# Kernel optimization log

Hardware: AMD Instinct MI355X
Metric: run time of the kernel (lower is better)

Reference implementation:

```python
import jax, jax.numpy as jnp
import numpy as np

DIM = 768
HEADS = 12
FF = 3072
EPS = 1e-6


def setup_inputs() -> dict:
    key = jax.random.key(0)
    ks = jax.random.split(key, 12)
    B, S, D, F_ = 64, 197, DIM, FF
    s = 0.02
    inp = {
        "x": jax.random.normal(ks[0], (B, S, D), jnp.float32),
        "Wq": jax.random.normal(ks[1], (D, D), jnp.float32) * s,
        "bq": jnp.zeros((D,), jnp.float32),
        "Wk": jax.random.normal(ks[2], (D, D), jnp.float32) * s,
        "bk": jnp.zeros((D,), jnp.float32),
        "Wv": jax.random.normal(ks[3], (D, D), jnp.float32) * s,
        "bv": jnp.zeros((D,), jnp.float32),
        "Wo": jax.random.normal(ks[4], (D, D), jnp.float32) * s,
        "bo": jnp.zeros((D,), jnp.float32),
        "ln1_w": jnp.ones((D,), jnp.float32),
        "ln1_b": jnp.zeros((D,), jnp.float32),
        "W1": jax.random.normal(ks[5], (D, F_), jnp.float32) * s,
        "b1": jnp.zeros((F_,), jnp.float32),
        "W2": jax.random.normal(ks[6], (F_, D), jnp.float32) * s,
        "b2": jnp.zeros((D,), jnp.float32),
        "ln2_w": jnp.ones((D,), jnp.float32),
        "ln2_b": jnp.zeros((D,), jnp.float32),
        "mask": jnp.ones((B, S), jnp.int32),
    }
    return inp


def _layernorm(x, w, b):
    m = jnp.mean(x, axis=-1, keepdims=True)
    v = jnp.mean(jnp.square(x - m), axis=-1, keepdims=True)  # unbiased=False
    return (x - m) / jnp.sqrt(v + EPS) * w + b


def _block(x, mask_f, Wq, bq, Wk, bk, Wv, bv, Wo, bo, ln1_w, ln1_b, W1, b1, W2, b2, ln2_w, ln2_b):
    B, S, D = x.shape
    H = HEADS
    Dh = D // H
    # --- attention (pre-norm) ---
    h = _layernorm(x, ln1_w, ln1_b)
    q = (h @ Wq + bq).reshape(B, S, H, Dh).transpose(0, 2, 1, 3)
    k = (h @ Wk + bk).reshape(B, S, H, Dh).transpose(0, 2, 1, 3)
    v = (h @ Wv + bv).reshape(B, S, H, Dh).transpose(0, 2, 1, 3)
    scores = jnp.einsum("bhqd,bhkd->bhqk", q, k) / jnp.sqrt(jnp.float32(Dh))
    scores = scores - 10000.0 * (1.0 - mask_f[:, None, None, :])
    probs = jax.nn.softmax(scores, axis=-1)
    attn = jnp.einsum("bhqk,bhkd->bhqd", probs, v).transpose(0, 2, 1, 3).reshape(B, S, D)
    x = x + (attn @ Wo + bo)  # dropout = identity (eval)
    # --- FFN (pre-norm), exact erf GELU (F.gelu default) ---
    h = _layernorm(x, ln2_w, ln2_b)
    h = jax.nn.gelu(h @ W1 + b1, approximate=False)
    x = x + (h @ W2 + b2)
    return x


def reference(x, Wq, bq, Wk, bk, Wv, bv, Wo, bo, ln1_w, ln1_b, W1, b1, W2, b2, ln2_w, ln2_b, mask):
    mask_f = mask.astype(jnp.float32)
    return _block(x, mask_f, Wq, bq, Wk, bk, Wv, bv, Wo, bo, ln1_w, ln1_b, W1, b1, W2, b2, ln2_w, ln2_b)
```

## Files before the change

### kernel.cpp

```cpp
#include <hip/hip_runtime.h>
#include <stdint.h>

#define B_   64
#define S_   197
#define D_   768
#define H_   12
#define F_   3072
#define BS_  (B_ * S_)

typedef __attribute__((ext_vector_type(8))) short short8;
typedef __attribute__((ext_vector_type(4))) float f32x4;

__device__ __forceinline__ float bf2f(unsigned short h) {
    union { unsigned int u; float f; } v; v.u = ((unsigned int)h) << 16; return v.f;
}
__device__ __forceinline__ unsigned short f2bf(float f) {
    union { float f; unsigned int u; } v; v.f = f;
    unsigned int r = v.u + 0x7FFFu + ((v.u >> 16) & 1u);
    return (unsigned short)(r >> 16);
}

__device__ __forceinline__ void g2l16(const void* g, void* l) {
    __builtin_amdgcn_global_load_lds(
        (const __attribute__((address_space(1))) unsigned int*)g,
        (__attribute__((address_space(3))) unsigned int*)l, 16, 0, 0);
}

__global__ __launch_bounds__(256)
void transpose_all(const float* __restrict__ Wq, const float* __restrict__ Wk,
                   const float* __restrict__ Wv, const float* __restrict__ Wo,
                   const float* __restrict__ W1, const float* __restrict__ W2,
                   const float* __restrict__ bq, const float* __restrict__ bk,
                   const float* __restrict__ bv,
                   unsigned short* __restrict__ wqkvT, unsigned short* __restrict__ woT,
                   unsigned short* __restrict__ w1T, unsigned short* __restrict__ w2T,
                   float* __restrict__ bcat) {
    int blk = blockIdx.x;
    int tx = threadIdx.x, ty = threadIdx.y;
    if (blk == 6912) {
        for (int i = ty * 32 + tx; i < 2304; i += 256)
            bcat[i] = i < 768 ? bq[i] : (i < 1536 ? bk[i - 768] : bv[i - 1536]);
        return;
    }
    const float* W; unsigned short* Wt; int K, N, rel, nx;
    if (blk < 2304) {
        int m = blk / 576; rel = blk - m * 576; K = 768; N = 768; nx = 24;
        W  = m == 0 ? Wq : m == 1 ? Wk : m == 2 ? Wv : Wo;
        Wt = m < 3 ? wqkvT + (size_t)m * 768 * 768 : woT;
    } else if (blk < 4608) {
        rel = blk - 2304; K = 768; N = 3072; nx = 96; W = W1; Wt = w1T;
    } else {
        rel = blk - 4608; K = 3072; N = 768; nx = 24; W = W2; Wt = w2T;
    }
    int n0 = (rel % nx) * 32, k0 = (rel / nx) * 32;
    __shared__ float t[32][33];
#pragma unroll
    for (int i = ty; i < 32; i += 8) t[i][tx] = W[(size_t)(k0 + i) * N + n0 + tx];
    __syncthreads();
#pragma unroll
    for (int i = ty; i < 32; i += 8) Wt[(size_t)(n0 + i) * K + k0 + tx] = f2bf(t[tx][i]);
}

__global__ __launch_bounds__(256)
void ln_kernel(const float* __restrict__ x, const float* __restrict__ w,
               const float* __restrict__ b, unsigned short* __restrict__ out) {
    int row = blockIdx.x; size_t base = (size_t)row * 768;
    int tid = threadIdx.x;
    float v0 = x[base + tid], v1 = x[base + tid + 256], v2 = x[base + tid + 512];
    float s1 = v0 + v1 + v2;
    float s2 = v0 * v0 + v1 * v1 + v2 * v2;
#pragma unroll
    for (int off = 32; off > 0; off >>= 1) { s1 += __shfl_xor(s1, off); s2 += __shfl_xor(s2, off); }
    __shared__ float sa[4], sb[4];
    int w4 = tid >> 6;
    if ((tid & 63) == 0) { sa[w4] = s1; sb[w4] = s2; }
    __syncthreads();
    s1 = sa[0] + sa[1] + sa[2] + sa[3];
    s2 = sb[0] + sb[1] + sb[2] + sb[3];
    float mean = s1 * (1.f / 768.f);
    float var  = s2 * (1.f / 768.f) - mean * mean;
    float rstd = rsqrtf(var + 1e-6f);
    out[base + tid]       = f2bf((v0 - mean) * rstd * w[tid]       + b[tid]);
    out[base + tid + 256] = f2bf((v1 - mean) * rstd * w[tid + 256] + b[tid + 256]);
    out[base + tid + 512] = f2bf((v2 - mean) * rstd * w[tid + 512] + b[tid + 512]);
}

template<int MODE>
__global__ __launch_bounds__(256)
void gemm_bf16(const unsigned short* __restrict__ A, const unsigned short* __restrict__ Bt,
               const float* __restrict__ bias, const float* __restrict__ resid,
               void* __restrict__ out, int M, int N, int K) {
    __shared__ unsigned short As[2][128 * 32];
    __shared__ unsigned short Bs[2][128 * 32];
    const int tid = threadIdx.x;
    const int l = tid & 63, w = tid >> 6;
    const int lr = l & 15, lg = l >> 4;
    const int wr = w >> 1, wc = w & 1;

    const int nMt = gridDim.y;
    const int nwg = gridDim.x * gridDim.y;
    const int orig = blockIdx.x + gridDim.x * blockIdx.y;
    const int q8 = nwg >> 3, r8 = nwg & 7;
    const int xcd = orig & 7, idx = orig >> 3;
    const int wgid = (xcd < r8 ? xcd * (q8 + 1) : r8 * (q8 + 1) + (xcd - r8) * q8) + idx;
    const int bm0 = (wgid % nMt) * 128;
    const int bn0 = (wgid / nMt) * 128;

    const int srow = l >> 2;
    const int sblk = (l & 3) ^ ((l >> 3) & 3);
    auto stage = [&](int buf, int k0) {
#pragma unroll
        for (int p = 0; p < 2; ++p) {
            int r0 = p * 64 + w * 16;
            int ra = bm0 + r0 + srow; ra = ra < M ? ra : M - 1;
            g2l16(A + (size_t)ra * K + k0 + sblk * 8, &As[buf][r0 * 32]);
            int rb = bn0 + r0 + srow;
            g2l16(Bt + (size_t)rb * K + k0 + sblk * 8, &Bs[buf][r0 * 32]);
        }
    };

    f32x4 acc[4][4];
#pragma unroll
    for (int i = 0; i < 4; ++i)
#pragma unroll
        for (int j = 0; j < 4; ++j) acc[i][j] = (f32x4){0.f, 0.f, 0.f, 0.f};

    stage(0, 0);
    __syncthreads();
    int cur = 0;
    const int NK = K >> 5;
    const int rblk = lg ^ ((lr >> 1) & 3);
    for (int kt = 0; kt < NK; ++kt) {
        if (kt + 1 < NK) stage(cur ^ 1, (kt + 1) << 5);
        short8 af[4], bfr[4];
#pragma unroll
        for (int i = 0; i < 4; ++i) af[i]  = *(const short8*)&As[cur][(wr * 64 + i * 16 + lr) * 32 + rblk * 8];
#pragma unroll
        for (int j = 0; j < 4; ++j) bfr[j] = *(const short8*)&Bs[cur][(wc * 64 + j * 16 + lr) * 32 + rblk * 8];
#pragma unroll
        for (int i = 0; i < 4; ++i)
#pragma unroll
            for (int j = 0; j < 4; ++j)
                acc[i][j] = __builtin_amdgcn_mfma_f32_16x16x32_bf16(af[i], bfr[j], acc[i][j], 0, 0, 0);
        __syncthreads();
        cur ^= 1;
    }
#pragma unroll
    for (int i = 0; i < 4; ++i)
#pragma unroll
        for (int j = 0; j < 4; ++j)
#pragma unroll
            for (int r = 0; r < 4; ++r) {
                int gm = bm0 + wr * 64 + i * 16 + lg * 4 + r;
                int gn = bn0 + wc * 64 + j * 16 + lr;
                if (gm < M) {
                    float c = acc[i][j][r] + bias[gn];
                    if (MODE == 0) {
                        if (gn < 768) c *= 0.125f;
                        ((unsigned short*)out)[(size_t)gm * N + gn] = f2bf(c);
                    } else if (MODE == 1) {
                        ((float*)out)[(size_t)gm * N + gn] = c + resid[(size_t)gm * N + gn];
                    } else {
                        float g = 0.5f * c * (1.f + erff(c * 0.70710678118f));
                        ((unsigned short*)out)[(size_t)gm * N + gn] = f2bf(g);
                    }
                }
            }
}

__global__ __launch_bounds__(256)
void attn_mfma(const unsigned short* __restrict__ qkv, const int* __restrict__ mask,
               unsigned short* __restrict__ ctx) {
    __shared__ unsigned short Ks[208 * 64];
    __shared__ unsigned short Vt[64 * 256];
    __shared__ unsigned short Psl[4][16 * 40];
    __shared__ float maskadj[224];
    const int bh = blockIdx.x, b = bh / 12, h = bh - b * 12;
    const int tid = threadIdx.x, l = tid & 63, w = tid >> 6;
    const int lr = l & 15, lg = l >> 4;
    const unsigned short* Qg = qkv + (size_t)b * 197 * 2304 + h * 64;
    const unsigned short* Kg = Qg + 768;
    const unsigned short* Vg = Qg + 1536;

    if (tid < 224)
        maskadj[tid] = tid < 197 ? -10000.f * (1.f - (float)mask[b * 197 + tid]) : -1e30f;

    for (int c = w; c < 26; c += 4) {
        int row = c * 8 + (l >> 3);
        int rc = row < 197 ? row : 196;
        int blk = (l & 7) ^ (row & 7);
        g2l16(Kg + (size_t)rc * 2304 + blk * 8, &Ks[c * 8 * 64]);
    }
    {
        int jj = tid >> 3, db = tid & 7;
#pragma unroll
        for (int it = 0; it < 7; ++it) {
            int j = it * 32 + jj;
            short8 v = (short8){0, 0, 0, 0, 0, 0, 0, 0};
            if (j < 197) v = *(const short8*)(Vg + (size_t)j * 2304 + db * 8);
#pragma unroll
            for (int e = 0; e < 8; ++e) {
                int d = db * 8 + e;
                Vt[d * 256 + (((j >> 3) ^ (d & 7)) * 8) + (j & 7)] = (unsigned short)v[e];
            }
        }
    }
    __syncthreads();

    for (int t = w; t < 13; t += 4) {
        const int q0 = t * 16;
        int qr = q0 + lr; qr = qr < 197 ? qr : 196;
        const short8 qf0 = *(const short8*)(Qg + (size_t)qr * 2304 + lg * 8);
        const short8 qf1 = *(const short8*)(Qg + (size_t)qr * 2304 + 32 + lg * 8);

        f32x4 sc[13];
#pragma unroll
        for (int kt = 0; kt < 13; ++kt) {
            const int krow = kt * 16 + lr;
            const short8 kf0 = *(const short8*)&Ks[krow * 64 + ((lg ^ (lr & 7)) * 8)];
            const short8 kf1 = *(const short8*)&Ks[krow * 64 + (((4 + lg) ^ (lr & 7)) * 8)];
            f32x4 a = (f32x4){0.f, 0.f, 0.f, 0.f};
            a = __builtin_amdgcn_mfma_f32_16x16x32_bf16(qf0, kf0, a, 0, 0, 0);
            a = __builtin_amdgcn_mfma_f32_16x16x32_bf16(qf1, kf1, a, 0, 0, 0);
            sc[kt] = a;
        }
        float mx[4] = {-1e30f, -1e30f, -1e30f, -1e30f};
#pragma unroll
        for (int kt = 0; kt < 13; ++kt) {
            float ma = maskadj[kt * 16 + lr];
#pragma unroll
            for (int r = 0; r < 4; ++r) {
                sc[kt][r] += ma;
                mx[r] = fmaxf(mx[r], sc[kt][r]);
            }
        }
#pragma unroll
        for (int r = 0; r < 4; ++r) {
            mx[r] = fmaxf(mx[r], __shfl_xor(mx[r], 1));
            mx[r] = fmaxf(mx[r], __shfl_xor(mx[r], 2));
            mx[r] = fmaxf(mx[r], __shfl_xor(mx[r], 4));
            mx[r] = fmaxf(mx[r], __shfl_xor(mx[r], 8));
        }
        float sm[4] = {0.f, 0.f, 0.f, 0.f};
#pragma unroll
        for (int kt = 0; kt < 13; ++kt)
#pragma unroll
            for (int r = 0; r < 4; ++r) {
                float p = __expf(sc[kt][r] - mx[r]);
                sc[kt][r] = p;
                sm[r] += p;
            }
#pragma unroll
        for (int r = 0; r < 4; ++r) {
            sm[r] += __shfl_xor(sm[r], 1);
            sm[r] += __shfl_xor(sm[r], 2);
            sm[r] += __shfl_xor(sm[r], 4);
            sm[r] += __shfl_xor(sm[r], 8);
            sm[r] = 1.f / sm[r];
        }
        f32x4 ao[4];
#pragma unroll
        for (int dt = 0; dt < 4; ++dt) ao[dt] = (f32x4){0.f, 0.f, 0.f, 0.f};
        unsigned short* Pw = &Psl[w][0];
#pragma unroll
        for (int ks = 0; ks < 7; ++ks) {
#pragma unroll
            for (int tl = 0; tl < 2; ++tl) {
                const int kt = ks * 2 + tl;
#pragma unroll
                for (int r = 0; r < 4; ++r) {
                    unsigned short pv = 0;
                    if (kt < 13) pv = f2bf(sc[kt][r] * sm[r]);
                    Pw[(lg * 4 + r) * 40 + tl * 16 + lr] = pv;
                }
            }
            const short8 pf = *(const short8*)&Pw[lr * 40 + lg * 8];
#pragma unroll
            for (int dt = 0; dt < 4; ++dt) {
                const int drow = dt * 16 + lr;
                const short8 vf = *(const short8*)&Vt[drow * 256 + (((4 * ks + lg) ^ (lr & 7)) * 8)];
                ao[dt] = __builtin_amdgcn_mfma_f32_16x16x32_bf16(vf, pf, ao[dt], 0, 0, 0);
            }
        }
        const int q = q0 + lr;
        if (q < 197) {
            unsigned short* crow = ctx + ((size_t)b * 197 + q) * 768 + h * 64;
#pragma unroll
            for (int dt = 0; dt < 4; ++dt) {
                union { unsigned short u[4]; uint2 v; } pk;
#pragma unroll
                for (int r = 0; r < 4; ++r) pk.u[r] = f2bf(ao[dt][r]);
                *(uint2*)(crow + dt * 16 + lg * 4) = pk.v;
            }
        }
    }
}

extern "C" void kernel_launch(void* const* d_in, const int* in_sizes, int n_in,
                              void* d_out, int out_size, void* d_ws, size_t ws_size,
                              hipStream_t stream) {
    const float* x    = (const float*)d_in[0];
    const float* Wq   = (const float*)d_in[1];
    const float* bq   = (const float*)d_in[2];
    const float* Wk   = (const float*)d_in[3];
    const float* bk   = (const float*)d_in[4];
    const float* Wv   = (const float*)d_in[5];
    const float* bv   = (const float*)d_in[6];
    const float* Wo   = (const float*)d_in[7];
    const float* bo   = (const float*)d_in[8];
    const float* ln1w = (const float*)d_in[9];
    const float* ln1b = (const float*)d_in[10];
    const float* W1   = (const float*)d_in[11];
    const float* b1   = (const float*)d_in[12];
    const float* W2   = (const float*)d_in[13];
    const float* b2   = (const float*)d_in[14];
    const float* ln2w = (const float*)d_in[15];
    const float* ln2b = (const float*)d_in[16];
    const int*   mask = (const int*)d_in[17];

    size_t off = 0;
    auto nxt = [&](size_t bytes) -> void* {
        void* r = (char*)d_ws + off; off += (bytes + 255) & ~(size_t)255; return r;
    };
    unsigned short* hbuf  = (unsigned short*)nxt((size_t)BS_ * 768 * 2);
    unsigned short* qkvg  = (unsigned short*)nxt((size_t)BS_ * 3072 * 2);
    unsigned short* wqkvT = (unsigned short*)nxt((size_t)2304 * 768 * 2);
    unsigned short* woT   = (unsigned short*)nxt((size_t)768 * 768 * 2);
    unsigned short* w1T   = (unsigned short*)nxt((size_t)3072 * 768 * 2);
    unsigned short* w2T   = (unsigned short*)nxt((size_t)768 * 3072 * 2);
    float*          bcat  = (float*)nxt(2304 * 4);
    unsigned short* ctx   = (unsigned short*)nxt((size_t)BS_ * 768 * 2);
    (void)ws_size; (void)in_sizes; (void)n_in; (void)out_size;

    transpose_all<<<6913, dim3(32, 8), 0, stream>>>(Wq, Wk, Wv, Wo, W1, W2, bq, bk, bv,
                                                    wqkvT, woT, w1T, w2T, bcat);
    ln_kernel<<<BS_, 256, 0, stream>>>(x, ln1w, ln1b, hbuf);
    gemm_bf16<0><<<dim3(18, 99), 256, 0, stream>>>(hbuf, wqkvT, bcat, nullptr, qkvg, BS_, 2304, 768);
    attn_mfma<<<768, 256, 0, stream>>>(qkvg, mask, ctx);
    gemm_bf16<1><<<dim3(6, 99), 256, 0, stream>>>(ctx, woT, bo, x, d_out, BS_, 768, 768);
    ln_kernel<<<BS_, 256, 0, stream>>>((const float*)d_out, ln2w, ln2b, hbuf);
    gemm_bf16<2><<<dim3(24, 99), 256, 0, stream>>>(hbuf, w1T, b1, nullptr, qkvg, BS_, 3072, 768);
    gemm_bf16<1><<<dim3(6, 99), 256, 0, stream>>>(qkvg, w2T, b2, (const float*)d_out, d_out, BS_, 768, 3072);
}
```

Before: 482.8 us.

## Replace 128x128 GEMM with 256x256 tile, 512-thread, BK=64 pipelined kernel

Replaces the 128x128x32 bf16 GEMM with a 256x256x64 tile kernel using 8 waves. Each wave computes 128x64 of the output, and global-to-LDS prefetch of the next K tile is interleaved with MFMA sub-steps, with priority hints and a wider XOR swizzle. Larger tiles are meant to raise data reuse and cut LDS and barrier overhead per FLOP. The cost is 128KB LDS per block, so only one block fits per CU despite launch_bounds(512,2). Grids also shrink (e.g. 150 blocks for the N=768 GEMMs), which can underfill 256 CUs. The exact erff in the FFN GELU epilogue is swapped for an Abramowitz-Stegun polynomial approximation.

```diff
diff --git a/kernel.cpp b/kernel.cpp
--- a/kernel.cpp
+++ b/kernel.cpp
@@ -24,6 +24,16 @@
     __builtin_amdgcn_global_load_lds(
         (const __attribute__((address_space(1))) unsigned int*)g,
         (__attribute__((address_space(3))) unsigned int*)l, 16, 0, 0);
+}
+
+__device__ __forceinline__ float gelu_f(float c) {
+    float z = fabsf(c) * 0.70710678118f;
+    float t = __builtin_amdgcn_rcpf(1.f + 0.3275911f * z);
+    float p = ((((1.061405429f * t - 1.453152027f) * t + 1.421413741f) * t
+               - 0.284496736f) * t + 0.254829592f) * t;
+    float erfv = 1.f - p * __expf(-z * z);
+    erfv = c < 0.f ? -erfv : erfv;
+    return 0.5f * c * (1.f + erfv);
 }
 
 __global__ __launch_bounds__(256)
@@ -86,16 +96,16 @@
 }
 
 template<int MODE>
-__global__ __launch_bounds__(256)
-void gemm_bf16(const unsigned short* __restrict__ A, const unsigned short* __restrict__ Bt,
-               const float* __restrict__ bias, const float* __restrict__ resid,
-               void* __restrict__ out, int M, int N, int K) {
-    __shared__ unsigned short As[2][128 * 32];
-    __shared__ unsigned short Bs[2][128 * 32];
+__global__ __launch_bounds__(512, 2)
+void gemm256(const unsigned short* __restrict__ A, const unsigned short* __restrict__ Bt,
+             const float* __restrict__ bias, const float* __restrict__ resid,
+             void* __restrict__ out, int M, int N, int K) {
+    __shared__ unsigned short As[2][256 * 64];
+    __shared__ unsigned short Bs[2][256 * 64];
     const int tid = threadIdx.x;
-    const int l = tid & 63, w = tid >> 6;
+    const int l = tid & 63, wid = tid >> 6;
     const int lr = l & 15, lg = l >> 4;
-    const int wr = w >> 1, wc = w & 1;
+    const int wr = wid >> 2, wc = wid & 3;
 
     const int nMt = gridDim.y;
     const int nwg = gridDim.x * gridDim.y;
@@ -103,66 +113,107 @@
     const int q8 = nwg >> 3, r8 = nwg & 7;
     const int xcd = orig & 7, idx = orig >> 3;
     const int wgid = (xcd < r8 ? xcd * (q8 + 1) : r8 * (q8 + 1) + (xcd - r8) * q8) + idx;
-    const int bm0 = (wgid % nMt) * 128;
-    const int bn0 = (wgid / nMt) * 128;
-
-    const int srow = l >> 2;
-    const int sblk = (l & 3) ^ ((l >> 3) & 3);
-    auto stage = [&](int buf, int k0) {
-#pragma unroll
-        for (int p = 0; p < 2; ++p) {
-            int r0 = p * 64 + w * 16;
-            int ra = bm0 + r0 + srow; ra = ra < M ? ra : M - 1;
-            g2l16(A + (size_t)ra * K + k0 + sblk * 8, &As[buf][r0 * 32]);
-            int rb = bn0 + r0 + srow;
-            g2l16(Bt + (size_t)rb * K + k0 + sblk * 8, &Bs[buf][r0 * 32]);
-        }
+    const int bm0 = (wgid % nMt) * 256;
+    const int bn0 = (wgid / nMt) * 256;
+
+    const int srow_lo = l >> 3;
+    const int slb = (l & 7) ^ (l >> 3);
+
+    auto stageChunk = [&](int buf, int kt, int c) {
+        int ca = c & 3;
+        int row = ca * 64 + wid * 8 + srow_lo;
+        unsigned short* dst;
+        const unsigned short* src;
+        if (c < 4) {
+            int gr = bm0 + row; gr = gr < M ? gr : M - 1;
+            src = A + (size_t)gr * K + kt * 64 + slb * 8;
+            dst = &As[buf][(ca * 512 + wid * 64) * 8];
+        } else {
+            int gr = bn0 + row;
+            src = Bt + (size_t)gr * K + kt * 64 + slb * 8;
+            dst = &Bs[buf][(ca * 512 + wid * 64) * 8];
+        }
+        g2l16(src, dst);
     };
 
-    f32x4 acc[4][4];
-#pragma unroll
-    for (int i = 0; i < 4; ++i)
+    f32x4 acc[8][4];
+#pragma unroll
+    for (int i = 0; i < 8; ++i)
 #pragma unroll
         for (int j = 0; j < 4; ++j) acc[i][j] = (f32x4){0.f, 0.f, 0.f, 0.f};
 
-    stage(0, 0);
-    __syncthreads();
-    int cur = 0;
-    const int NK = K >> 5;
-    const int rblk = lg ^ ((lr >> 1) & 3);
+    const int NK = K >> 6;
+#pragma unroll
+    for (int c = 0; c < 8; ++c) stageChunk(0, 0, c);
+    asm volatile("s_waitcnt vmcnt(0)" ::: "memory");
+    __builtin_amdgcn_s_barrier();
+
+    const int rsw = lr & 7;
     for (int kt = 0; kt < NK; ++kt) {
-        if (kt + 1 < NK) stage(cur ^ 1, (kt + 1) << 5);
-        short8 af[4], bfr[4];
-#pragma unroll
-        for (int i = 0; i < 4; ++i) af[i]  = *(const short8*)&As[cur][(wr * 64 + i * 16 + lr) * 32 + rblk * 8];
-#pragma unroll
-        for (int j = 0; j < 4; ++j) bfr[j] = *(const short8*)&Bs[cur][(wc * 64 + j * 16 + lr) * 32 + rblk * 8];
-#pragma unroll
-        for (int i = 0; i < 4; ++i)
-#pragma unroll
-            for (int j = 0; j < 4; ++j)
-                acc[i][j] = __builtin_amdgcn_mfma_f32_16x16x32_bf16(af[i], bfr[j], acc[i][j], 0, 0, 0);
-        __syncthreads();
-        cur ^= 1;
-    }
-#pragma unroll
-    for (int i = 0; i < 4; ++i)
-#pragma unroll
-        for (int j = 0; j < 4; ++j)
+        const int buf = kt & 1;
+        const bool pf = (kt + 1 < NK);
+        short8 bfr[4][2];
+#pragma unroll
+        for (int q = 0; q < 4; ++q) {
+            if (q == 0) {
+#pragma unroll
+                for (int nt = 0; nt < 4; ++nt)
+#pragma unroll
+                    for (int kk = 0; kk < 2; ++kk)
+                        bfr[nt][kk] = *(const short8*)&Bs[buf][(wc * 64 + nt * 16 + lr) * 64 +
+                                                              (((kk * 4 + lg) ^ rsw) * 8)];
+            }
+            short8 af[2][2];
+#pragma unroll
+            for (int tmt = 0; tmt < 2; ++tmt)
+#pragma unroll
+                for (int kk = 0; kk < 2; ++kk)
+                    af[tmt][kk] = *(const short8*)&As[buf][(wr * 128 + (q * 2 + tmt) * 16 + lr) * 64 +
+                                                          (((kk * 4 + lg) ^ rsw) * 8)];
+            if (pf && q == 0) {
+#pragma unroll
+                for (int c = 0; c < 4; ++c) stageChunk(buf ^ 1, kt + 1, c);
+            }
+            if (pf && q == 1) {
+#pragma unroll
+                for (int c = 4; c < 8; ++c) stageChunk(buf ^ 1, kt + 1, c);
+            }
+            asm volatile("s_waitcnt lgkmcnt(0)" ::: "memory");
+            __builtin_amdgcn_sched_barrier(0);
+            __builtin_amdgcn_s_setprio(1);
+#pragma unroll
+            for (int tmt = 0; tmt < 2; ++tmt)
+#pragma unroll
+                for (int nt = 0; nt < 4; ++nt)
+#pragma unroll
+                    for (int kk = 0; kk < 2; ++kk)
+                        acc[q * 2 + tmt][nt] = __builtin_amdgcn_mfma_f32_16x16x32_bf16(
+                            af[tmt][kk], bfr[nt][kk], acc[q * 2 + tmt][nt], 0, 0, 0);
+            __builtin_amdgcn_s_setprio(0);
+        }
+        if (pf) {
+            asm volatile("s_waitcnt vmcnt(0)" ::: "memory");
+            __builtin_amdgcn_s_barrier();
+        }
+    }
+
+#pragma unroll
+    for (int mt = 0; mt < 8; ++mt)
+#pragma unroll
+        for (int nt = 0; nt < 4; ++nt)
 #pragma unroll
             for (int r = 0; r < 4; ++r) {
-                int gm = bm0 + wr * 64 + i * 16 + lg * 4 + r;
-                int gn = bn0 + wc * 64 + j * 16 + lr;
+                int gm = bm0 + wr * 128 + mt * 16 + lg * 4 + r;
+                int gn = bn0 + wc * 64 + nt * 16 + lr;
                 if (gm < M) {
-                    float c = acc[i][j][r] + bias[gn];
+                    float c = acc[mt][nt][r] + bias[gn];
                     if (MODE == 0) {
                         if (gn < 768) c *= 0.125f;
                         ((unsigned short*)out)[(size_t)gm * N + gn] = f2bf(c);
                     } else if (MODE == 1) {
                         ((float*)out)[(size_t)gm * N + gn] = c + resid[(size_t)gm * N + gn];
                     } else {
-                        float g = 0.5f * c * (1.f + erff(c * 0.70710678118f));
-                        ((unsigned short*)out)[(size_t)gm * N + gn] = f2bf(g);
+                        ((unsigned short*)out)[(size_t)gm * N + gn] = f2bf(gelu_f(c));
                     }
                 }
             }
@@ -335,10 +386,10 @@
     transpose_all<<<6913, dim3(32, 8), 0, stream>>>(Wq, Wk, Wv, Wo, W1, W2, bq, bk, bv,
                                                     wqkvT, woT, w1T, w2T, bcat);
     ln_kernel<<<BS_, 256, 0, stream>>>(x, ln1w, ln1b, hbuf);
-    gemm_bf16<0><<<dim3(18, 99), 256, 0, stream>>>(hbuf, wqkvT, bcat, nullptr, qkvg, BS_, 2304, 768);
+    gemm256<0><<<dim3(9, 50), 512, 0, stream>>>(hbuf, wqkvT, bcat, nullptr, qkvg, BS_, 2304, 768);
     attn_mfma<<<768, 256, 0, stream>>>(qkvg, mask, ctx);
-    gemm_bf16<1><<<dim3(6, 99), 256, 0, stream>>>(ctx, woT, bo, x, d_out, BS_, 768, 768);
+    gemm256<1><<<dim3(3, 50), 512, 0, stream>>>(ctx, woT, bo, x, d_out, BS_, 768, 768);
     ln_kernel<<<BS_, 256, 0, stream>>>((const float*)d_out, ln2w, ln2b, hbuf);
-    gemm_bf16<2><<<dim3(24, 99), 256, 0, stream>>>(hbuf, w1T, b1, nullptr, qkvg, BS_, 3072, 768);
-    gemm_bf16<1><<<dim3(6, 99), 256, 0, stream>>>(qkvg, w2T, b2, (const float*)d_out, d_out, BS_, 768, 3072);
-}
+    gemm256<2><<<dim3(12, 50), 512, 0, stream>>>(hbuf, w1T, b1, nullptr, qkvg, BS_, 3072, 768);
+    gemm256<1><<<dim3(3, 50), 512, 0, stream>>>(qkvg, w2T, b2, (const float*)d_out, d_out, BS_, 768, 3072);
+}
```

New measurement: 485.4 us. About the same (+0.5%).

## Deepen GEMM pipeline to 4-stage LDS ring with manual waitcnt and faster GELU

Applied to the files above, without the earlier changes.

Replaces the double-buffered GEMM with a 4-deep LDS ring that keeps three tiles in flight, using explicit vmcnt waits and a single barrier per k-step instead of two syncthreads. It also raises MFMA issue priority, remaps workgroup order so consecutive workgroups walk along N, and swaps erff for a polynomial erf approximation in the GELU epilogue. This doubles LDS use to 64KB per block, which may cap occupancy, and the polynomial erf adds small approximation error.

```diff
diff --git a/kernel.cpp b/kernel.cpp
--- a/kernel.cpp
+++ b/kernel.cpp
@@ -24,6 +24,16 @@
     __builtin_amdgcn_global_load_lds(
         (const __attribute__((address_space(1))) unsigned int*)g,
         (__attribute__((address_space(3))) unsigned int*)l, 16, 0, 0);
+}
+
+__device__ __forceinline__ float gelu_f(float c) {
+    float z = fabsf(c) * 0.70710678118f;
+    float t = __builtin_amdgcn_rcpf(1.f + 0.3275911f * z);
+    float p = ((((1.061405429f * t - 1.453152027f) * t + 1.421413741f) * t
+               - 0.284496736f) * t + 0.254829592f) * t;
+    float erfv = 1.f - p * __expf(-z * z);
+    erfv = c < 0.f ? -erfv : erfv;
+    return 0.5f * c * (1.f + erfv);
 }
 
 __global__ __launch_bounds__(256)
@@ -86,36 +96,37 @@
 }
 
 template<int MODE>
-__global__ __launch_bounds__(256)
-void gemm_bf16(const unsigned short* __restrict__ A, const unsigned short* __restrict__ Bt,
-               const float* __restrict__ bias, const float* __restrict__ resid,
-               void* __restrict__ out, int M, int N, int K) {
-    __shared__ unsigned short As[2][128 * 32];
-    __shared__ unsigned short Bs[2][128 * 32];
+__global__ __launch_bounds__(256, 2)
+void gemm128(const unsigned short* __restrict__ A, const unsigned short* __restrict__ Bt,
+             const float* __restrict__ bias, const float* __restrict__ resid,
+             void* __restrict__ out, int M, int N, int K) {
+    __shared__ unsigned short As[4][128 * 32];
+    __shared__ unsigned short Bs[4][128 * 32];
     const int tid = threadIdx.x;
     const int l = tid & 63, w = tid >> 6;
     const int lr = l & 15, lg = l >> 4;
     const int wr = w >> 1, wc = w & 1;
 
-    const int nMt = gridDim.y;
+    const int nNt = gridDim.x;
     const int nwg = gridDim.x * gridDim.y;
     const int orig = blockIdx.x + gridDim.x * blockIdx.y;
     const int q8 = nwg >> 3, r8 = nwg & 7;
     const int xcd = orig & 7, idx = orig >> 3;
     const int wgid = (xcd < r8 ? xcd * (q8 + 1) : r8 * (q8 + 1) + (xcd - r8) * q8) + idx;
-    const int bm0 = (wgid % nMt) * 128;
-    const int bn0 = (wgid / nMt) * 128;
+    const int bn0 = (wgid % nNt) * 128;
+    const int bm0 = (wgid / nNt) * 128;
 
     const int srow = l >> 2;
     const int sblk = (l & 3) ^ ((l >> 3) & 3);
-    auto stage = [&](int buf, int k0) {
+    auto stage = [&](int ring, int kt) {
+        const int k0 = kt << 5;
 #pragma unroll
         for (int p = 0; p < 2; ++p) {
             int r0 = p * 64 + w * 16;
             int ra = bm0 + r0 + srow; ra = ra < M ? ra : M - 1;
-            g2l16(A + (size_t)ra * K + k0 + sblk * 8, &As[buf][r0 * 32]);
+            g2l16(A + (size_t)ra * K + k0 + sblk * 8, &As[ring][r0 * 32]);
             int rb = bn0 + r0 + srow;
-            g2l16(Bt + (size_t)rb * K + k0 + sblk * 8, &Bs[buf][r0 * 32]);
+            g2l16(Bt + (size_t)rb * K + k0 + sblk * 8, &Bs[ring][r0 * 32]);
         }
     };
 
@@ -125,26 +136,34 @@
 #pragma unroll
         for (int j = 0; j < 4; ++j) acc[i][j] = (f32x4){0.f, 0.f, 0.f, 0.f};
 
-    stage(0, 0);
-    __syncthreads();
-    int cur = 0;
     const int NK = K >> 5;
+    stage(0, 0); stage(1, 1); stage(2, 2);
+
     const int rblk = lg ^ ((lr >> 1) & 3);
     for (int kt = 0; kt < NK; ++kt) {
-        if (kt + 1 < NK) stage(cur ^ 1, (kt + 1) << 5);
+        if (kt + 3 < NK)      asm volatile("s_waitcnt vmcnt(8)" ::: "memory");
+        else if (kt + 2 < NK) asm volatile("s_waitcnt vmcnt(4)" ::: "memory");
+        else                  asm volatile("s_waitcnt vmcnt(0)" ::: "memory");
+        __builtin_amdgcn_s_barrier();
+        if (kt + 3 < NK) stage((kt + 3) & 3, kt + 3);
+        const unsigned short* Ab = &As[kt & 3][0];
+        const unsigned short* Bb = &Bs[kt & 3][0];
         short8 af[4], bfr[4];
 #pragma unroll
-        for (int i = 0; i < 4; ++i) af[i]  = *(const short8*)&As[cur][(wr * 64 + i * 16 + lr) * 32 + rblk * 8];
-#pragma unroll
-        for (int j = 0; j < 4; ++j) bfr[j] = *(const short8*)&Bs[cur][(wc * 64 + j * 16 + lr) * 32 + rblk * 8];
+        for (int i = 0; i < 4; ++i) af[i]  = *(const short8*)&Ab[(wr * 64 + i * 16 + lr) * 32 + rblk * 8];
+#pragma unroll
+        for (int j = 0; j < 4; ++j) bfr[j] = *(const short8*)&Bb[(wc * 64 + j * 16 + lr) * 32 + rblk * 8];
+        asm volatile("s_waitcnt lgkmcnt(0)" ::: "memory");
+        __builtin_amdgcn_sched_barrier(0);
+        __builtin_amdgcn_s_setprio(1);
 #pragma unroll
         for (int i = 0; i < 4; ++i)
 #pragma unroll
             for (int j = 0; j < 4; ++j)
                 acc[i][j] = __builtin_amdgcn_mfma_f32_16x16x32_bf16(af[i], bfr[j], acc[i][j], 0, 0, 0);
-        __syncthreads();
-        cur ^= 1;
-    }
+        __builtin_amdgcn_s_setprio(0);
+    }
+
 #pragma unroll
     for (int i = 0; i < 4; ++i)
 #pragma unroll
@@ -161,8 +180,7 @@
                     } else if (MODE == 1) {
                         ((float*)out)[(size_t)gm * N + gn] = c + resid[(size_t)gm * N + gn];
                     } else {
-                        float g = 0.5f * c * (1.f + erff(c * 0.70710678118f));
-                        ((unsigned short*)out)[(size_t)gm * N + gn] = f2bf(g);
+                        ((unsigned short*)out)[(size_t)gm * N + gn] = f2bf(gelu_f(c));
                     }
                 }
             }
@@ -335,10 +353,10 @@
     transpose_all<<<6913, dim3(32, 8), 0, stream>>>(Wq, Wk, Wv, Wo, W1, W2, bq, bk, bv,
                                                     wqkvT, woT, w1T, w2T, bcat);
     ln_kernel<<<BS_, 256, 0, stream>>>(x, ln1w, ln1b, hbuf);
-    gemm_bf16<0><<<dim3(18, 99), 256, 0, stream>>>(hbuf, wqkvT, bcat, nullptr, qkvg, BS_, 2304, 768);
+    gemm128<0><<<dim3(18, 99), 256, 0, stream>>>(hbuf, wqkvT, bcat, nullptr, qkvg, BS_, 2304, 768);
     attn_mfma<<<768, 256, 0, stream>>>(qkvg, mask, ctx);
-    gemm_bf16<1><<<dim3(6, 99), 256, 0, stream>>>(ctx, woT, bo, x, d_out, BS_, 768, 768);
+    gemm128<1><<<dim3(6, 99), 256, 0, stream>>>(ctx, woT, bo, x, d_out, BS_, 768, 768);
     ln_kernel<<<BS_, 256, 0, stream>>>((const float*)d_out, ln2w, ln2b, hbuf);
-    gemm_bf16<2><<<dim3(24, 99), 256, 0, stream>>>(hbuf, w1T, b1, nullptr, qkvg, BS_, 3072, 768);
-    gemm_bf16<1><<<dim3(6, 99), 256, 0, stream>>>(qkvg, w2T, b2, (const float*)d_out, d_out, BS_, 768, 3072);
-}
+    gemm128<2><<<dim3(24, 99), 256, 0, stream>>>(hbuf, w1T, b1, nullptr, qkvg, BS_, 3072, 768);
+    gemm128<1><<<dim3(6, 99), 256, 0, stream>>>(qkvg, w2T, b2, (const float*)d_out, d_out, BS_, 768, 3072);
+}
```

Result: slower. 560.8 us (+16.2%).
